# Performance work log

Hardware: AMD Instinct MI355X
Metric: run time of the kernel (lower is better)

Reference implementation:

```python
import jax, jax.numpy as jnp
import numpy as np

D, E, N, DD, K = 1024, 2048, 16, 64, 4  # d_model, d_inner, d_state, dt_rank, d_conv
B, L = 2, 1024
EPS = 1e-5


def setup_inputs() -> dict:
    key = jax.random.key(0)
    ks = jax.random.split(key, 12)
    f = lambda k, s, scale=0.02: (jax.random.normal(k, s, jnp.float32) * scale)
    return dict(
        resid=jax.random.normal(ks[0], (B, L, D), jnp.float32),
        workplace_h=jnp.zeros((B, E, N), jnp.float32),
        norm_w=jnp.ones((D,), jnp.float32),
        skip_w=f(ks[1], (E, D)),
        in_w=f(ks[2], (E, D)),
        conv_w=f(ks[3], (E, 1, K), 0.2),
        conv_b=jnp.zeros((E,), jnp.float32),
        wd1=f(ks[4], (DD, E)),
        wd2_w=f(ks[5], (E, DD)),
        wd2_b=jnp.zeros((E,), jnp.float32),
        wb=f(ks[6], (N, E)),
        wc=f(ks[7], (N, E)),
        A_log=f(ks[8], (E, N), 1.0),
        W_D=jnp.ones((E,), jnp.float32),
        out_w=f(ks[9], (D, E)),
    )


def reference(resid, workplace_h, norm_w, skip_w, in_w, conv_w, conv_b,
              wd1, wd2_w, wd2_b, wb, wc, A_log, W_D, out_w):
    # RMSNorm
    x = resid * jax.lax.rsqrt(jnp.mean(resid ** 2, -1, keepdims=True) + EPS) * norm_w
    skip = x @ skip_w.T                      # [B,L,E]
    xi = x @ in_w.T                          # [B,L,E]
    # depthwise causal conv1d (torch pads both sides then slices to L; equivalent to left-pad K-1)
    xc = jnp.swapaxes(xi, 1, 2)              # [B,E,L]
    xc = jax.lax.conv_general_dilated(
        xc, conv_w, window_strides=(1,), padding=[(K - 1, 0)],
        feature_group_count=E, dimension_numbers=('NCH', 'OIH', 'NCH'))
    xc = xc + conv_b[None, :, None]
    x2 = jax.nn.silu(jnp.swapaxes(xc, 1, 2))  # [B,L,E]

    A = -jnp.exp(A_log)                       # [E,N]
    delta = jax.nn.softplus((x2 @ wd1.T) @ wd2_w.T + wd2_b)   # [B,L,E]
    A_bar = jnp.exp(delta[..., None] * A)                      # [B,L,E,N]
    Bm = x2 @ wb.T                                             # [B,L,N]
    B_bar = delta[..., None] * Bm[:, :, None, :]               # [B,L,E,N]
    Cm = x2 @ wc.T                                             # [B,L,N]

    def step(h, inp):
        a, b_, xl, cl = inp                   # [B,E,N],[B,E,N],[B,E],[B,N]
        h = a * h + b_ * xl[..., None]
        y = jnp.einsum('ben,bn->be', h, cl)
        return h, y

    h0 = jnp.zeros_like(workplace_h)          # workplace_h is zeroed (h[:] = 0)
    xs = (jnp.swapaxes(A_bar, 0, 1), jnp.swapaxes(B_bar, 0, 1),
          jnp.swapaxes(x2, 0, 1), jnp.swapaxes(Cm, 0, 1))
    _, ys = jax.lax.scan(step, h0, xs)        # ys: [L,B,E]
    y = jnp.swapaxes(ys, 0, 1)                # [B,L,E]

    y = (y + x2 * W_D) * jax.nn.silu(skip)
    return resid + y @ out_w.T
```

## Files before the change

kernel.cpp:

```cpp
#include <hip/hip_runtime.h>
#include <math.h>

#define Dm 1024
#define Em 2048
#define Nm 16
#define DDm 64
#define Bb 2
#define Lm 1024
#define Mrows (Bb*Lm)
#define NCH 32
#define CLEN 32
#define KS 16
#define KSO 4

typedef __attribute__((ext_vector_type(8))) short bf16x8;
typedef __attribute__((ext_vector_type(4))) float f32x4;
typedef unsigned int u32;
typedef unsigned short u16;

__device__ __forceinline__ u16 f2bf(float f) {
    union { float f; u32 u; } v; v.f = f;
    u32 r = v.u + 0x7fffu + ((v.u >> 16) & 1u);
    return (u16)(r >> 16);
}

__device__ __forceinline__ void async_copy16(const void* g, void* l) {
    __builtin_amdgcn_global_load_lds(
        (const __attribute__((address_space(1))) u32*)g,
        (__attribute__((address_space(3))) u32*)l,
        16, 0, 0);
}

__global__ __launch_bounds__(256) void rmsnorm_kernel(const float* __restrict__ resid,
                                                      const float* __restrict__ w,
                                                      u16* __restrict__ x) {
    int row = blockIdx.x;
    const float* r = resid + (size_t)row * Dm;
    float s = 0.f;
    for (int i = threadIdx.x; i < Dm; i += 256) { float v = r[i]; s += v * v; }
    __shared__ float red[4];
    for (int off = 32; off; off >>= 1) s += __shfl_down(s, off, 64);
    if ((threadIdx.x & 63) == 0) red[threadIdx.x >> 6] = s;
    __syncthreads();
    if (threadIdx.x == 0) {
        float t = red[0] + red[1] + red[2] + red[3];
        red[0] = rsqrtf(t / (float)Dm + 1e-5f);
    }
    __syncthreads();
    float sc = red[0];
    u16* xo = x + (size_t)row * Dm;
    for (int i = threadIdx.x; i < Dm; i += 256) xo[i] = f2bf(r[i] * sc * w[i]);
}

__global__ __launch_bounds__(256) void prep_all_kernel(const float* __restrict__ skip_w,
                                                       const float* __restrict__ in_w,
                                                       const float* __restrict__ out_w,
                                                       const float* __restrict__ wd2_w,
                                                       const float* __restrict__ wb,
                                                       const float* __restrict__ wc,
                                                       const float* __restrict__ wd1,
                                                       u16* __restrict__ skip_w_bf,
                                                       u16* __restrict__ in_w_bf,
                                                       u16* __restrict__ out_w_bf,
                                                       u16* __restrict__ wd2_bf,
                                                       u16* __restrict__ wtb) {
    const int R0 = 2097152, R1 = 4194304, R2 = 6291456, R3 = 6422528, R4 = 6684672;
    int i = blockIdx.x * 256 + threadIdx.x;
    if (i < R0) skip_w_bf[i] = f2bf(skip_w[i]);
    else if (i < R1) in_w_bf[i - R0] = f2bf(in_w[i - R0]);
    else if (i < R2) out_w_bf[i - R1] = f2bf(out_w[i - R1]);
    else if (i < R3) wd2_bf[i - R2] = f2bf(wd2_w[i - R2]);
    else if (i < R4) {
        int j = i - R3;
        int c = j >> 11, k = j & 2047;
        float v = 0.f;
        if (c < 16) v = wb[(size_t)c * Em + k];
        else if (c < 32) v = wc[(size_t)(c - 16) * Em + k];
        else if (c < 96) v = wd1[(size_t)(c - 32) * Em + k];
        wtb[j] = f2bf(v);
    }
}

__global__ __launch_bounds__(256) void gemm_db(const u16* __restrict__ A,
                                               const u16* __restrict__ W,
                                               const float* __restrict__ bias,
                                               float* __restrict__ C,
                                               float* __restrict__ C2, int split,
                                               int M, int N, int lda, int klen, int act) {
    __shared__ __align__(16) u16 As[2][128 * 32];
    __shared__ __align__(16) u16 Ws[2][64 * 32];
    int tid = threadIdx.x;
    int lane = tid & 63, wave = tid >> 6;
    int bm = blockIdx.y * 128, bn = blockIdx.x * 64;
    int kbase = blockIdx.z * klen;
    int lm = lane & 15, lq = lane >> 4;
    int wm = (wave & 1) * 64, wn = (wave >> 1) * 32;

    f32x4 acc[4][2] = {};
    int ldrow = lane >> 2;
    int gchunk = ((lane & 3) ^ ((lane >> 3) & 3)) * 8;
    int psw = (lm >> 1) & 3;
    int rdoff = (lq ^ psw) * 8;

    const u16* Arow0 = A + (size_t)(bm + wave * 16 + ldrow) * lda + gchunk;
    const u16* Arow1 = A + (size_t)(bm + 64 + wave * 16 + ldrow) * lda + gchunk;
    const u16* Wrow  = W + (size_t)(bn + wave * 16 + ldrow) * lda + gchunk;
    int ldsA = (wave * 16) * 32;
    int ldsA2 = (64 + wave * 16) * 32;
    int ldsW = (wave * 16) * 32;

    int nIter = klen / 32;
    async_copy16(Arow0 + kbase, &As[0][ldsA]);
    async_copy16(Arow1 + kbase, &As[0][ldsA2]);
    async_copy16(Wrow + kbase, &Ws[0][ldsW]);
    __syncthreads();

    for (int it = 0; it < nIter; ++it) {
        int cur = it & 1, nxt = cur ^ 1;
        if (it + 1 < nIter) {
            int k0 = kbase + (it + 1) * 32;
            async_copy16(Arow0 + k0, &As[nxt][ldsA]);
            async_copy16(Arow1 + k0, &As[nxt][ldsA2]);
            async_copy16(Wrow + k0, &Ws[nxt][ldsW]);
        }
        bf16x8 a[4], b[2];
        #pragma unroll
        for (int mi = 0; mi < 4; ++mi)
            a[mi] = *(const bf16x8*)&As[cur][(wm + mi * 16 + lm) * 32 + rdoff];
        #pragma unroll
        for (int nj = 0; nj < 2; ++nj)
            b[nj] = *(const bf16x8*)&Ws[cur][(wn + nj * 16 + lm) * 32 + rdoff];
        #pragma unroll
        for (int mi = 0; mi < 4; ++mi)
            #pragma unroll
            for (int nj = 0; nj < 2; ++nj)
                acc[mi][nj] = __builtin_amdgcn_mfma_f32_16x16x32_bf16(a[mi], b[nj], acc[mi][nj], 0, 0, 0);
        __syncthreads();
    }

    int ldc = C2 ? split : N;
    float* Cz = C + (size_t)blockIdx.z * M * ldc;
    #pragma unroll
    for (int nj = 0; nj < 2; ++nj) {
        int col = bn + wn + nj * 16 + lm;
        float bv = bias ? bias[col] : 0.f;
        float* Cp = Cz; int colw = col;
        if (C2 && col >= split) { Cp = C2; colw = col - split; }
        #pragma unroll
        for (int mi = 0; mi < 4; ++mi) {
            #pragma unroll
            for (int r = 0; r < 4; ++r) {
                int row = bm + wm + mi * 16 + lq * 4 + r;
                float v = acc[mi][nj][r] + bv;
                if (act == 1) v = (v > 20.f) ? v : log1pf(expf(v));
                Cp[(size_t)row * ldc + colw] = v;
            }
        }
    }
}

__global__ __launch_bounds__(256) void out_reduce_kernel(const float* __restrict__ part,
                                                         const float* __restrict__ resid,
                                                         float* __restrict__ out) {
    int idx = blockIdx.x * 256 + threadIdx.x;
    const float4* r4 = (const float4*)resid;
    const float4* p4 = (const float4*)part;
    float4 s = r4[idx];
    const int plane = Mrows * Dm / 4;
    #pragma unroll
    for (int ks = 0; ks < KSO; ++ks) {
        float4 p = p4[(size_t)ks * plane + idx];
        s.x += p.x; s.y += p.y; s.z += p.z; s.w += p.w;
    }
    ((float4*)out)[idx] = s;
}

__global__ __launch_bounds__(256) void small_reduce_kernel(const float* __restrict__ Cp,
                                                           float* __restrict__ Bm,
                                                           float* __restrict__ Cm,
                                                           u16* __restrict__ d1) {
    int idx = blockIdx.x * 256 + threadIdx.x;
    int row = idx >> 7, col = idx & 127;
    float s = 0.f;
    #pragma unroll
    for (int ks = 0; ks < KS; ++ks) s += Cp[(size_t)ks * (Mrows * 128) + idx];
    if (col < 16) Bm[(size_t)row * 16 + col] = s;
    else if (col < 32) Cm[(size_t)row * 16 + (col - 16)] = s;
    else if (col < 96) d1[(size_t)row * 64 + (col - 32)] = f2bf(s);
}

__global__ __launch_bounds__(256) void conv_silu_kernel(const float* __restrict__ xi,
                                                        const float* __restrict__ cw,
                                                        const float* __restrict__ cb,
                                                        float* __restrict__ x2,
                                                        u16* __restrict__ x2b, int total) {
    int idx = blockIdx.x * 256 + threadIdx.x;
    if (idx >= total) return;
    int e = idx & (Em - 1);
    int l = (idx >> 11) & (Lm - 1);
    const float* base = xi + idx;
    float w0 = cw[e * 4 + 0], w1 = cw[e * 4 + 1], w2 = cw[e * 4 + 2], w3 = cw[e * 4 + 3];
    float acc = cb[e];
    if (l >= 3) acc += w0 * base[-3 * Em];
    if (l >= 2) acc += w1 * base[-2 * Em];
    if (l >= 1) acc += w2 * base[-1 * Em];
    acc += w3 * base[0];
    float v = acc / (1.f + __expf(-acc));
    x2[idx] = v;
    x2b[idx] = f2bf(v);
}

__global__ __launch_bounds__(256) void scan1_kernel(const float* __restrict__ delta,
                                                    const float* __restrict__ x2,
                                                    const float* __restrict__ Bm,
                                                    const float* __restrict__ A_log,
                                                    float* __restrict__ h_end,
                                                    float* __restrict__ P) {
    int e = (blockIdx.x & 7) * 256 + threadIdx.x;
    int bc = blockIdx.x >> 3;
    int b = bc & 1, c = bc >> 1;
    float A[16];
    {
        const float4* al = (const float4*)(A_log + e * 16);
        float4 q0 = al[0], q1 = al[1], q2 = al[2], q3 = al[3];
        A[0]=-expf(q0.x); A[1]=-expf(q0.y); A[2]=-expf(q0.z); A[3]=-expf(q0.w);
        A[4]=-expf(q1.x); A[5]=-expf(q1.y); A[6]=-expf(q1.z); A[7]=-expf(q1.w);
        A[8]=-expf(q2.x); A[9]=-expf(q2.y); A[10]=-expf(q2.z); A[11]=-expf(q2.w);
        A[12]=-expf(q3.x); A[13]=-expf(q3.y); A[14]=-expf(q3.z); A[15]=-expf(q3.w);
    }
    float h[16], Pr[16];
    #pragma unroll
    for (int k = 0; k < 16; ++k) { h[k] = 0.f; Pr[k] = 1.f; }

    int l0 = c * CLEN;
    const float* dp = delta + ((size_t)(b * Lm + l0)) * Em + e;
    const float* xp = x2    + ((size_t)(b * Lm + l0)) * Em + e;
    const float* bp = Bm    + ((size_t)(b * Lm + l0)) * Nm;

    float d_n = dp[0], x_n = xp[0];
    float4 b0n = *(const float4*)(bp + 0), b1n = *(const float4*)(bp + 4);
    float4 b2n = *(const float4*)(bp + 8), b3n = *(const float4*)(bp + 12);

    #pragma unroll 1
    for (int l = 0; l < CLEN; ++l) {
        float d = d_n, xv = x_n;
        float4 b0 = b0n, b1 = b1n, b2 = b2n, b3 = b3n;
        if (l < CLEN - 1) {
            d_n = dp[(size_t)(l + 1) * Em]; x_n = xp[(size_t)(l + 1) * Em];
            const float* nb = bp + (size_t)(l + 1) * Nm;
            b0n = *(const float4*)(nb); b1n = *(const float4*)(nb + 4);
            b2n = *(const float4*)(nb + 8); b3n = *(const float4*)(nb + 12);
        }
        float dx = d * xv;
        float bb[16] = {b0.x,b0.y,b0.z,b0.w, b1.x,b1.y,b1.z,b1.w,
                        b2.x,b2.y,b2.z,b2.w, b3.x,b3.y,b3.z,b3.w};
        #pragma unroll
        for (int k = 0; k < 16; ++k) {
            float a = __expf(d * A[k]);
            h[k] = a * h[k] + bb[k] * dx;
            Pr[k] *= a;
        }
    }
    size_t base = (((size_t)c * 2 + b) * 16) * 2048 + e;
    #pragma unroll
    for (int k = 0; k < 16; ++k) {
        h_end[base + k * 2048] = h[k];
        P[base + k * 2048] = Pr[k];
    }
}

__global__ __launch_bounds__(256) void scan2_kernel(float* __restrict__ h_end,
                                                    const float* __restrict__ P) {
    int T = blockIdx.x * 256 + threadIdx.x;
    float hi = 0.f;
    float he_n = h_end[T], p_n = P[T];
    #pragma unroll 1
    for (int c = 0; c < NCH; ++c) {
        float he = he_n, p = p_n;
        if (c < NCH - 1) {
            he_n = h_end[(size_t)(c + 1) * 65536 + T];
            p_n  = P[(size_t)(c + 1) * 65536 + T];
        }
        float hnew = fmaf(p, hi, he);
        h_end[(size_t)c * 65536 + T] = hi;
        hi = hnew;
    }
}

__global__ __launch_bounds__(256) void scan3_kernel(const float* __restrict__ delta,
                                                    const float* __restrict__ x2,
                                                    const float* __restrict__ Bm,
                                                    const float* __restrict__ Cm,
                                                    const float* __restrict__ A_log,
                                                    const float* __restrict__ h_init,
                                                    const float* __restrict__ skip,
                                                    const float* __restrict__ W_D,
                                                    u16* __restrict__ yb) {
    int e = (blockIdx.x & 7) * 256 + threadIdx.x;
    int bc = blockIdx.x >> 3;
    int b = bc & 1, c = bc >> 1;
    float A[16];
    {
        const float4* al = (const float4*)(A_log + e * 16);
        float4 q0 = al[0], q1 = al[1], q2 = al[2], q3 = al[3];
        A[0]=-expf(q0.x); A[1]=-expf(q0.y); A[2]=-expf(q0.z); A[3]=-expf(q0.w);
        A[4]=-expf(q1.x); A[5]=-expf(q1.y); A[6]=-expf(q1.z); A[7]=-expf(q1.w);
        A[8]=-expf(q2.x); A[9]=-expf(q2.y); A[10]=-expf(q2.z); A[11]=-expf(q2.w);
        A[12]=-expf(q3.x); A[13]=-expf(q3.y); A[14]=-expf(q3.z); A[15]=-expf(q3.w);
    }
    float h[16];
    {
        size_t base = (((size_t)c * 2 + b) * 16) * 2048 + e;
        #pragma unroll
        for (int k = 0; k < 16; ++k) h[k] = h_init[base + k * 2048];
    }
    float wd = W_D[e];

    int l0 = c * CLEN;
    const float* dp = delta + ((size_t)(b * Lm + l0)) * Em + e;
    const float* xp = x2    + ((size_t)(b * Lm + l0)) * Em + e;
    const float* sp = skip  + ((size_t)(b * Lm + l0)) * Em + e;
    const float* bp = Bm    + ((size_t)(b * Lm + l0)) * Nm;
    const float* cp = Cm    + ((size_t)(b * Lm + l0)) * Nm;
    u16* yp = yb + ((size_t)(b * Lm + l0)) * Em + e;

    float d_n = dp[0], x_n = xp[0], s_n = sp[0];
    float4 b0n = *(const float4*)(bp + 0), b1n = *(const float4*)(bp + 4);
    float4 b2n = *(const float4*)(bp + 8), b3n = *(const float4*)(bp + 12);
    float4 c0n = *(const float4*)(cp + 0), c1n = *(const float4*)(cp + 4);
    float4 c2n = *(const float4*)(cp + 8), c3n = *(const float4*)(cp + 12);

    #pragma unroll 1
    for (int l = 0; l < CLEN; ++l) {
        float d = d_n, xv = x_n, sv = s_n;
        float4 b0 = b0n, b1 = b1n, b2 = b2n, b3 = b3n;
        float4 c0 = c0n, c1 = c1n, c2 = c2n, c3 = c3n;
        if (l < CLEN - 1) {
            d_n = dp[(size_t)(l + 1) * Em]; x_n = xp[(size_t)(l + 1) * Em];
            s_n = sp[(size_t)(l + 1) * Em];
            const float* nb = bp + (size_t)(l + 1) * Nm;
            b0n = *(const float4*)(nb); b1n = *(const float4*)(nb + 4);
            b2n = *(const float4*)(nb + 8); b3n = *(const float4*)(nb + 12);
            const float* nc = cp + (size_t)(l + 1) * Nm;
            c0n = *(const float4*)(nc); c1n = *(const float4*)(nc + 4);
            c2n = *(const float4*)(nc + 8); c3n = *(const float4*)(nc + 12);
        }
        float dx = d * xv;
        float bb[16] = {b0.x,b0.y,b0.z,b0.w, b1.x,b1.y,b1.z,b1.w,
                        b2.x,b2.y,b2.z,b2.w, b3.x,b3.y,b3.z,b3.w};
        float cc[16] = {c0.x,c0.y,c0.z,c0.w, c1.x,c1.y,c1.z,c1.w,
                        c2.x,c2.y,c2.z,c2.w, c3.x,c3.y,c3.z,c3.w};
        float yv = 0.f;
        #pragma unroll
        for (int k = 0; k < 16; ++k) {
            float a = __expf(d * A[k]);
            h[k] = a * h[k] + bb[k] * dx;
            yv += h[k] * cc[k];
        }
        float sig = 1.f / (1.f + __expf(-sv));
        yp[(size_t)l * Em] = f2bf((yv + xv * wd) * (sv * sig));
    }
}

extern "C" void kernel_launch(void* const* d_in, const int* in_sizes, int n_in,
                              void* d_out, int out_size, void* d_ws, size_t ws_size,
                              hipStream_t stream) {
    const float* resid  = (const float*)d_in[0];
    const float* norm_w = (const float*)d_in[2];
    const float* skip_w = (const float*)d_in[3];
    const float* in_w   = (const float*)d_in[4];
    const float* conv_w = (const float*)d_in[5];
    const float* conv_b = (const float*)d_in[6];
    const float* wd1    = (const float*)d_in[7];
    const float* wd2_w  = (const float*)d_in[8];
    const float* wd2_b  = (const float*)d_in[9];
    const float* wb     = (const float*)d_in[10];
    const float* wc     = (const float*)d_in[11];
    const float* A_log  = (const float*)d_in[12];
    const float* W_D    = (const float*)d_in[13];
    const float* out_w  = (const float*)d_in[14];
    float* out = (float*)d_out;

    float* ws = (float*)d_ws;
    float* region0 = ws; ws += 3 * 1024 * 1024;
    u16* x_bf      = (u16*)region0;
    u16* skip_w_bf = (u16*)(region0 + 1024 * 1024);
    u16* in_w_bf   = (u16*)(region0 + 2 * 1024 * 1024);
    float* h_endb  = region0;
    u16* out_w_bf  = (u16*)ws; ws += 1024 * 1024;
    u16* wd2_bf    = (u16*)ws; ws += 65536;
    u16* d1_bf     = (u16*)ws; ws += 65536;
    u16* wtb       = (u16*)ws; ws += 131072;
    float* Pbuf    = ws; ws += 2 * 1024 * 1024;
    float* Cpart   = ws; ws += (size_t)KS * Mrows * 128;
    float* skip    = ws; ws += (size_t)Mrows * Em;
    float* xi      = ws; ws += (size_t)Mrows * Em;
    float* x2      = ws; ws += (size_t)Mrows * Em;
    u16* x2_bf     = (u16*)ws; ws += (size_t)Mrows * Em / 2;
    u16* yb_bf     = (u16*)ws; ws += (size_t)Mrows * Em / 2;
    float* Bmb     = ws; ws += (size_t)Mrows * Nm;
    float* Cmb     = ws; ws += (size_t)Mrows * Nm;
    float* delta   = xi;
    float* OutPart = skip;

    const int M = Mrows;

    prep_all_kernel<<<6684672 / 256, 256, 0, stream>>>(
        skip_w, in_w, out_w, wd2_w, wb, wc, wd1,
        skip_w_bf, in_w_bf, out_w_bf, wd2_bf, wtb);

    rmsnorm_kernel<<<M, 256, 0, stream>>>(resid, norm_w, x_bf);

    gemm_db<<<dim3(2 * Em / 64, M / 128, 1), 256, 0, stream>>>(
        x_bf, skip_w_bf, nullptr, skip, xi, Em, M, 2 * Em, Dm, Dm, 0);

    conv_silu_kernel<<<(M * Em) / 256, 256, 0, stream>>>(xi, conv_w, conv_b, x2, x2_bf, M * Em);

    gemm_db<<<dim3(128 / 64, M / 128, KS), 256, 0, stream>>>(
        x2_bf, wtb, nullptr, Cpart, nullptr, 0, M, 128, Em, Em / KS, 0);
    small_reduce_kernel<<<(M * 128) / 256, 256, 0, stream>>>(Cpart, Bmb, Cmb, d1_bf);

    gemm_db<<<dim3(Em / 64, M / 128, 1), 256, 0, stream>>>(
        d1_bf, wd2_bf, wd2_b, delta, nullptr, 0, M, Em, DDm, DDm, 1);

    scan1_kernel<<<Bb * NCH * 8, 256, 0, stream>>>(delta, x2, Bmb, A_log, h_endb, Pbuf);
    scan2_kernel<<<65536 / 256, 256, 0, stream>>>(h_endb, Pbuf);
    scan3_kernel<<<Bb * NCH * 8, 256, 0, stream>>>(delta, x2, Bmb, Cmb, A_log, h_endb,
                                                   skip, W_D, yb_bf);

    gemm_db<<<dim3(Dm / 64, M / 128, KSO), 256, 0, stream>>>(
        yb_bf, out_w_bf, nullptr, OutPart, nullptr, 0, M, Dm, Em, Em / KSO, 0);
    out_reduce_kernel<<<(M * Dm / 4) / 256, 256, 0, stream>>>(OutPart, resid, out);
}
```

Measured before the change: 274.0 us.

## Merge prep and RMSNorm, widen input GEMM tile, drop fp32 x2 buffer

Folds the weight bf16 conversion and RMSNorm into one launch, with blocks split by index. The skip/in projection gets a new GEMM variant using 128x128 tiles (4x4 MFMA per wave) to improve operand reuse. The fp32 x2 activation is removed, so the scans read the bf16 copy, cutting memory traffic. In exchange, scan inputs lose precision, and the larger tile uses more registers and LDS, which may lower occupancy.

Measured after the change: 279.6 us. +2.0%, slower.

```diff
diff --git a/kernel.cpp b/kernel.cpp
--- a/kernel.cpp
+++ b/kernel.cpp
@@ -12,6 +12,7 @@
 #define CLEN 32
 #define KS 16
 #define KSO 4
+#define PREPB 26112
 
 typedef __attribute__((ext_vector_type(8))) short bf16x8;
 typedef __attribute__((ext_vector_type(4))) float f32x4;
@@ -22,6 +23,9 @@
     union { float f; u32 u; } v; v.f = f;
     u32 r = v.u + 0x7fffu + ((v.u >> 16) & 1u);
     return (u16)(r >> 16);
+}
+__device__ __forceinline__ float bf2f(u16 v) {
+    union { u32 u; float f; } t; t.u = ((u32)v) << 16; return t.f;
 }
 
 __device__ __forceinline__ void async_copy16(const void* g, void* l) {
@@ -31,10 +35,40 @@
         16, 0, 0);
 }
 
-__global__ __launch_bounds__(256) void rmsnorm_kernel(const float* __restrict__ resid,
-                                                      const float* __restrict__ w,
-                                                      u16* __restrict__ x) {
-    int row = blockIdx.x;
+__global__ __launch_bounds__(256) void prep_rms_kernel(const float* __restrict__ skip_w,
+                                                       const float* __restrict__ in_w,
+                                                       const float* __restrict__ out_w,
+                                                       const float* __restrict__ wd2_w,
+                                                       const float* __restrict__ wb,
+                                                       const float* __restrict__ wc,
+                                                       const float* __restrict__ wd1,
+                                                       const float* __restrict__ resid,
+                                                       const float* __restrict__ norm_w,
+                                                       u16* __restrict__ skip_w_bf,
+                                                       u16* __restrict__ in_w_bf,
+                                                       u16* __restrict__ out_w_bf,
+                                                       u16* __restrict__ wd2_bf,
+                                                       u16* __restrict__ wtb,
+                                                       u16* __restrict__ x) {
+    if (blockIdx.x < PREPB) {
+        const int R0 = 2097152, R1 = 4194304, R2 = 6291456, R3 = 6422528, R4 = 6684672;
+        int i = blockIdx.x * 256 + threadIdx.x;
+        if (i < R0) skip_w_bf[i] = f2bf(skip_w[i]);
+        else if (i < R1) in_w_bf[i - R0] = f2bf(in_w[i - R0]);
+        else if (i < R2) out_w_bf[i - R1] = f2bf(out_w[i - R1]);
+        else if (i < R3) wd2_bf[i - R2] = f2bf(wd2_w[i - R2]);
+        else if (i < R4) {
+            int j = i - R3;
+            int c = j >> 11, k = j & 2047;
+            float v = 0.f;
+            if (c < 16) v = wb[(size_t)c * Em + k];
+            else if (c < 32) v = wc[(size_t)(c - 16) * Em + k];
+            else if (c < 96) v = wd1[(size_t)(c - 32) * Em + k];
+            wtb[j] = f2bf(v);
+        }
+        return;
+    }
+    int row = blockIdx.x - PREPB;
     const float* r = resid + (size_t)row * Dm;
     float s = 0.f;
     for (int i = threadIdx.x; i < Dm; i += 256) { float v = r[i]; s += v * v; }
@@ -49,35 +83,85 @@
     __syncthreads();
     float sc = red[0];
     u16* xo = x + (size_t)row * Dm;
-    for (int i = threadIdx.x; i < Dm; i += 256) xo[i] = f2bf(r[i] * sc * w[i]);
-}
-
-__global__ __launch_bounds__(256) void prep_all_kernel(const float* __restrict__ skip_w,
-                                                       const float* __restrict__ in_w,
-                                                       const float* __restrict__ out_w,
-                                                       const float* __restrict__ wd2_w,
-                                                       const float* __restrict__ wb,
-                                                       const float* __restrict__ wc,
-                                                       const float* __restrict__ wd1,
-                                                       u16* __restrict__ skip_w_bf,
-                                                       u16* __restrict__ in_w_bf,
-                                                       u16* __restrict__ out_w_bf,
-                                                       u16* __restrict__ wd2_bf,
-                                                       u16* __restrict__ wtb) {
-    const int R0 = 2097152, R1 = 4194304, R2 = 6291456, R3 = 6422528, R4 = 6684672;
-    int i = blockIdx.x * 256 + threadIdx.x;
-    if (i < R0) skip_w_bf[i] = f2bf(skip_w[i]);
-    else if (i < R1) in_w_bf[i - R0] = f2bf(in_w[i - R0]);
-    else if (i < R2) out_w_bf[i - R1] = f2bf(out_w[i - R1]);
-    else if (i < R3) wd2_bf[i - R2] = f2bf(wd2_w[i - R2]);
-    else if (i < R4) {
-        int j = i - R3;
-        int c = j >> 11, k = j & 2047;
-        float v = 0.f;
-        if (c < 16) v = wb[(size_t)c * Em + k];
-        else if (c < 32) v = wc[(size_t)(c - 16) * Em + k];
-        else if (c < 96) v = wd1[(size_t)(c - 32) * Em + k];
-        wtb[j] = f2bf(v);
+    for (int i = threadIdx.x; i < Dm; i += 256) xo[i] = f2bf(r[i] * sc * norm_w[i]);
+}
+
+
+__global__ __launch_bounds__(256) void gemm_db2(const u16* __restrict__ A,
+                                                const u16* __restrict__ W,
+                                                const float* __restrict__ bias,
+                                                float* __restrict__ C,
+                                                float* __restrict__ C2, int split,
+                                                int M, int N, int lda, int klen, int act) {
+    __shared__ __align__(16) u16 As[2][128 * 32];
+    __shared__ __align__(16) u16 Ws[2][128 * 32];
+    int tid = threadIdx.x;
+    int lane = tid & 63, wave = tid >> 6;
+    int bm = blockIdx.y * 128, bn = blockIdx.x * 128;
+    int kbase = blockIdx.z * klen;
+    int lm = lane & 15, lq = lane >> 4;
+    int wm = (wave & 1) * 64, wn = (wave >> 1) * 64;
+
+    f32x4 acc[4][4] = {};
+    int ldrow = lane >> 2;
+    int gchunk = ((lane & 3) ^ ((lane >> 3) & 3)) * 8;
+    int rdoff = (lq ^ ((lm >> 1) & 3)) * 8;
+
+    const u16* Ar0 = A + (size_t)(bm + wave * 16 + ldrow) * lda + gchunk;
+    const u16* Ar1 = A + (size_t)(bm + 64 + wave * 16 + ldrow) * lda + gchunk;
+    const u16* Wr0 = W + (size_t)(bn + wave * 16 + ldrow) * lda + gchunk;
+    const u16* Wr1 = W + (size_t)(bn + 64 + wave * 16 + ldrow) * lda + gchunk;
+    int lds0 = (wave * 16) * 32, lds1 = (64 + wave * 16) * 32;
+
+    int nIter = klen / 32;
+    async_copy16(Ar0 + kbase, &As[0][lds0]);
+    async_copy16(Ar1 + kbase, &As[0][lds1]);
+    async_copy16(Wr0 + kbase, &Ws[0][lds0]);
+    async_copy16(Wr1 + kbase, &Ws[0][lds1]);
+    __syncthreads();
+
+    for (int it = 0; it < nIter; ++it) {
+        int cur = it & 1, nxt = cur ^ 1;
+        if (it + 1 < nIter) {
+            int k0 = kbase + (it + 1) * 32;
+            async_copy16(Ar0 + k0, &As[nxt][lds0]);
+            async_copy16(Ar1 + k0, &As[nxt][lds1]);
+            async_copy16(Wr0 + k0, &Ws[nxt][lds0]);
+            async_copy16(Wr1 + k0, &Ws[nxt][lds1]);
+        }
+        bf16x8 a[4], b[4];
+        #pragma unroll
+        for (int mi = 0; mi < 4; ++mi)
+            a[mi] = *(const bf16x8*)&As[cur][(wm + mi * 16 + lm) * 32 + rdoff];
+        #pragma unroll
+        for (int nj = 0; nj < 4; ++nj)
+            b[nj] = *(const bf16x8*)&Ws[cur][(wn + nj * 16 + lm) * 32 + rdoff];
+        #pragma unroll
+        for (int mi = 0; mi < 4; ++mi)
+            #pragma unroll
+            for (int nj = 0; nj < 4; ++nj)
+                acc[mi][nj] = __builtin_amdgcn_mfma_f32_16x16x32_bf16(a[mi], b[nj], acc[mi][nj], 0, 0, 0);
+        __syncthreads();
+    }
+
+    int ldc = C2 ? split : N;
+    float* Cz = C + (size_t)blockIdx.z * M * ldc;
+    #pragma unroll
+    for (int nj = 0; nj < 4; ++nj) {
+        int col = bn + wn + nj * 16 + lm;
+        float bv = bias ? bias[col] : 0.f;
+        float* Cp = Cz; int colw = col;
+        if (C2 && col >= split) { Cp = C2; colw = col - split; }
+        #pragma unroll
+        for (int mi = 0; mi < 4; ++mi) {
+            #pragma unroll
+            for (int r = 0; r < 4; ++r) {
+                int row = bm + wm + mi * 16 + lq * 4 + r;
+                float v = acc[mi][nj][r] + bv;
+                if (act == 1) v = (v > 20.f) ? v : log1pf(expf(v));
+                Cp[(size_t)row * ldc + colw] = v;
+            }
+        }
     }
 }
 
@@ -99,20 +183,18 @@
     f32x4 acc[4][2] = {};
     int ldrow = lane >> 2;
     int gchunk = ((lane & 3) ^ ((lane >> 3) & 3)) * 8;
-    int psw = (lm >> 1) & 3;
-    int rdoff = (lq ^ psw) * 8;
+    int rdoff = (lq ^ ((lm >> 1) & 3)) * 8;
 
     const u16* Arow0 = A + (size_t)(bm + wave * 16 + ldrow) * lda + gchunk;
     const u16* Arow1 = A + (size_t)(bm + 64 + wave * 16 + ldrow) * lda + gchunk;
     const u16* Wrow  = W + (size_t)(bn + wave * 16 + ldrow) * lda + gchunk;
     int ldsA = (wave * 16) * 32;
     int ldsA2 = (64 + wave * 16) * 32;
-    int ldsW = (wave * 16) * 32;
 
     int nIter = klen / 32;
     async_copy16(Arow0 + kbase, &As[0][ldsA]);
     async_copy16(Arow1 + kbase, &As[0][ldsA2]);
-    async_copy16(Wrow + kbase, &Ws[0][ldsW]);
+    async_copy16(Wrow + kbase, &Ws[0][ldsA]);
     __syncthreads();
 
     for (int it = 0; it < nIter; ++it) {
@@ -121,7 +203,7 @@
             int k0 = kbase + (it + 1) * 32;
             async_copy16(Arow0 + k0, &As[nxt][ldsA]);
             async_copy16(Arow1 + k0, &As[nxt][ldsA2]);
-            async_copy16(Wrow + k0, &Ws[nxt][ldsW]);
+            async_copy16(Wrow + k0, &Ws[nxt][ldsA]);
         }
         bf16x8 a[4], b[2];
         #pragma unroll
@@ -192,7 +274,6 @@
 __global__ __launch_bounds__(256) void conv_silu_kernel(const float* __restrict__ xi,
                                                         const float* __restrict__ cw,
                                                         const float* __restrict__ cb,
-                                                        float* __restrict__ x2,
                                                         u16* __restrict__ x2b, int total) {
     int idx = blockIdx.x * 256 + threadIdx.x;
     if (idx >= total) return;
@@ -206,12 +287,11 @@
     if (l >= 1) acc += w2 * base[-1 * Em];
     acc += w3 * base[0];
     float v = acc / (1.f + __expf(-acc));
-    x2[idx] = v;
     x2b[idx] = f2bf(v);
 }
 
 __global__ __launch_bounds__(256) void scan1_kernel(const float* __restrict__ delta,
-                                                    const float* __restrict__ x2,
+                                                    const u16* __restrict__ x2b,
                                                     const float* __restrict__ Bm,
                                                     const float* __restrict__ A_log,
                                                     float* __restrict__ h_end,
@@ -234,10 +314,10 @@
 
     int l0 = c * CLEN;
     const float* dp = delta + ((size_t)(b * Lm + l0)) * Em + e;
-    const float* xp = x2    + ((size_t)(b * Lm + l0)) * Em + e;
+    const u16* xp  = x2b   + ((size_t)(b * Lm + l0)) * Em + e;
     const float* bp = Bm    + ((size_t)(b * Lm + l0)) * Nm;
 
-    float d_n = dp[0], x_n = xp[0];
+    float d_n = dp[0], x_n = bf2f(xp[0]);
     float4 b0n = *(const float4*)(bp + 0), b1n = *(const float4*)(bp + 4);
     float4 b2n = *(const float4*)(bp + 8), b3n = *(const float4*)(bp + 12);
 
@@ -246,7 +326,7 @@
         float d = d_n, xv = x_n;
         float4 b0 = b0n, b1 = b1n, b2 = b2n, b3 = b3n;
         if (l < CLEN - 1) {
-            d_n = dp[(size_t)(l + 1) * Em]; x_n = xp[(size_t)(l + 1) * Em];
+            d_n = dp[(size_t)(l + 1) * Em]; x_n = bf2f(xp[(size_t)(l + 1) * Em]);
             const float* nb = bp + (size_t)(l + 1) * Nm;
             b0n = *(const float4*)(nb); b1n = *(const float4*)(nb + 4);
             b2n = *(const float4*)(nb + 8); b3n = *(const float4*)(nb + 12);
@@ -288,7 +368,7 @@
 }
 
 __global__ __launch_bounds__(256) void scan3_kernel(const float* __restrict__ delta,
-                                                    const float* __restrict__ x2,
+                                                    const u16* __restrict__ x2b,
                                                     const float* __restrict__ Bm,
                                                     const float* __restrict__ Cm,
                                                     const float* __restrict__ A_log,
@@ -318,13 +398,13 @@
 
     int l0 = c * CLEN;
     const float* dp = delta + ((size_t)(b * Lm + l0)) * Em + e;
-    const float* xp = x2    + ((size_t)(b * Lm + l0)) * Em + e;
+    const u16* xp  = x2b   + ((size_t)(b * Lm + l0)) * Em + e;
     const float* sp = skip  + ((size_t)(b * Lm + l0)) * Em + e;
     const float* bp = Bm    + ((size_t)(b * Lm + l0)) * Nm;
     const float* cp = Cm    + ((size_t)(b * Lm + l0)) * Nm;
     u16* yp = yb + ((size_t)(b * Lm + l0)) * Em + e;
 
-    float d_n = dp[0], x_n = xp[0], s_n = sp[0];
+    float d_n = dp[0], x_n = bf2f(xp[0]), s_n = sp[0];
     float4 b0n = *(const float4*)(bp + 0), b1n = *(const float4*)(bp + 4);
     float4 b2n = *(const float4*)(bp + 8), b3n = *(const float4*)(bp + 12);
     float4 c0n = *(const float4*)(cp + 0), c1n = *(const float4*)(cp + 4);
@@ -336,7 +416,7 @@
         float4 b0 = b0n, b1 = b1n, b2 = b2n, b3 = b3n;
         float4 c0 = c0n, c1 = c1n, c2 = c2n, c3 = c3n;
         if (l < CLEN - 1) {
-            d_n = dp[(size_t)(l + 1) * Em]; x_n = xp[(size_t)(l + 1) * Em];
+            d_n = dp[(size_t)(l + 1) * Em]; x_n = bf2f(xp[(size_t)(l + 1) * Em]);
             s_n = sp[(size_t)(l + 1) * Em];
             const float* nb = bp + (size_t)(l + 1) * Nm;
             b0n = *(const float4*)(nb); b1n = *(const float4*)(nb + 4);
@@ -395,7 +475,6 @@
     float* Cpart   = ws; ws += (size_t)KS * Mrows * 128;
     float* skip    = ws; ws += (size_t)Mrows * Em;
     float* xi      = ws; ws += (size_t)Mrows * Em;
-    float* x2      = ws; ws += (size_t)Mrows * Em;
     u16* x2_bf     = (u16*)ws; ws += (size_t)Mrows * Em / 2;
     u16* yb_bf     = (u16*)ws; ws += (size_t)Mrows * Em / 2;
     float* Bmb     = ws; ws += (size_t)Mrows * Nm;
@@ -405,16 +484,14 @@
 
     const int M = Mrows;
 
-    prep_all_kernel<<<6684672 / 256, 256, 0, stream>>>(
-        skip_w, in_w, out_w, wd2_w, wb, wc, wd1,
-        skip_w_bf, in_w_bf, out_w_bf, wd2_bf, wtb);
-
-    rmsnorm_kernel<<<M, 256, 0, stream>>>(resid, norm_w, x_bf);
-
-    gemm_db<<<dim3(2 * Em / 64, M / 128, 1), 256, 0, stream>>>(
+    prep_rms_kernel<<<PREPB + M, 256, 0, stream>>>(
+        skip_w, in_w, out_w, wd2_w, wb, wc, wd1, resid, norm_w,
+        skip_w_bf, in_w_bf, out_w_bf, wd2_bf, wtb, x_bf);
+
+    gemm_db2<<<dim3(2 * Em / 128, M / 128, 1), 256, 0, stream>>>(
         x_bf, skip_w_bf, nullptr, skip, xi, Em, M, 2 * Em, Dm, Dm, 0);
 
-    conv_silu_kernel<<<(M * Em) / 256, 256, 0, stream>>>(xi, conv_w, conv_b, x2, x2_bf, M * Em);
+    conv_silu_kernel<<<(M * Em) / 256, 256, 0, stream>>>(xi, conv_w, conv_b, x2_bf, M * Em);
 
     gemm_db<<<dim3(128 / 64, M / 128, KS), 256, 0, stream>>>(
         x2_bf, wtb, nullptr, Cpart, nullptr, 0, M, 128, Em, Em / KS, 0);
@@ -423,9 +500,9 @@
     gemm_db<<<dim3(Em / 64, M / 128, 1), 256, 0, stream>>>(
         d1_bf, wd2_bf, wd2_b, delta, nullptr, 0, M, Em, DDm, DDm, 1);
 
-    scan1_kernel<<<Bb * NCH * 8, 256, 0, stream>>>(delta, x2, Bmb, A_log, h_endb, Pbuf);
+    scan1_kernel<<<Bb * NCH * 8, 256, 0, stream>>>(delta, x2_bf, Bmb, A_log, h_endb, Pbuf);
     scan2_kernel<<<65536 / 256, 256, 0, stream>>>(h_endb, Pbuf);
-    scan3_kernel<<<Bb * NCH * 8, 256, 0, stream>>>(delta, x2, Bmb, Cmb, A_log, h_endb,
+    scan3_kernel<<<Bb * NCH * 8, 256, 0, stream>>>(delta, x2_bf, Bmb, Cmb, A_log, h_endb,
                                                    skip, W_D, yb_bf);
 
     gemm_db<<<dim3(Dm / 64, M / 128, KSO), 256, 0, stream>>>(
```
